# Optimization experiments

Measured on AMD Instinct MI355X. Metric: run time of the kernel, lower is better.

The kernel has to match this reference:

```python
import jax, jax.numpy as jnp
import numpy as np

IMG_W, IMG_H = 960.0, 512.0   # image_size (w, h)
HM_W, HM_H = 240, 128         # heatmap_size (w, h)


def _bilinear(fmap, gx, gy):
    # fmap: [C,H,W]; gx, gy: [N] normalized coords; bilinear, align_corners=False, zero padding
    C, H, W = fmap.shape
    ix = (gx + 1.0) * W * 0.5 - 0.5
    iy = (gy + 1.0) * H * 0.5 - 0.5
    x0f = jnp.floor(ix); y0f = jnp.floor(iy)
    wx1 = ix - x0f; wy1 = iy - y0f

    def tap(xf, yf, wgt):
        valid = (xf >= 0) & (xf <= W - 1) & (yf >= 0) & (yf <= H - 1)
        xc = jnp.clip(xf.astype(jnp.int32), 0, W - 1)
        yc = jnp.clip(yf.astype(jnp.int32), 0, H - 1)
        return fmap[:, yc, xc] * (wgt * valid.astype(fmap.dtype))

    return (tap(x0f, y0f, (1 - wx1) * (1 - wy1)) + tap(x0f + 1, y0f, wx1 * (1 - wy1))
            + tap(x0f, y0f + 1, (1 - wx1) * wy1) + tap(x0f + 1, y0f + 1, wx1 * wy1))


def _forward(feature_maps, grid_center, space_center, space_size, sub_space_size,
             cube, centers, trans, cam_R, cam_T, cam_f, cam_c):
    n_cam, B, C, H, W = feature_maps.shape
    vox = jnp.float32(cube)
    fine_n = (space_size / sub_space_size * (vox - 1.0)).astype(jnp.int32) + 1   # [3]
    fine_nf = fine_n.astype(jnp.float32)
    scale = (fine_nf - 1.0) / space_size
    bias = (-sub_space_size / 2.0 / space_size * (fine_nf - 1.0)
            - scale * (space_center - space_size / 2.0))
    centers_tl = jnp.round(grid_center[:, :3] * scale + bias).astype(jnp.int32)  # [B,3]
    offset = (centers_tl.astype(jnp.float32) / (fine_nf - 1.0) * space_size
              - space_size / 2.0 + sub_space_size / 2.0)                          # [B,3]
    mask_xy = jnp.maximum(((1.0 - grid_center[:, 5:7]) / 2.0 * (vox - 1.0)).astype(jnp.int32), 0)
    mask = jnp.concatenate([mask_xy, jnp.zeros((B, 1), jnp.int32)], axis=1)       # [B,3]
    start = jnp.maximum(centers_tl + mask, 0)
    end = jnp.minimum(centers_tl + cube - mask, fine_n)
    end = jnp.maximum(end, start + 1)

    # fixed-size sub-cube of fine-grid indices; out-of-window cells are masked to 0
    v = jnp.arange(cube)
    mesh = jnp.stack(jnp.meshgrid(v, v, v, indexing="ij"), axis=-1).reshape(-1, 3)  # [N,3]
    fidx = centers_tl[:, None, :] + mesh[None]                                       # [B,N,3]
    valid = jnp.all((fidx >= start[:, None, :]) & (fidx < end[:, None, :]), axis=-1)  # [B,N]
    valid = valid & (grid_center[:, 3:4] >= 0)
    world = (space_center - space_size / 2.0
             + fidx.astype(jnp.float32) / (fine_nf - 1.0) * space_size)              # [B,N,3]

    # pinhole world->pixel per (batch, camera)
    rel = world[:, None, :, :] - cam_T[:, :, None, :]                                # [B,K,N,3]
    Xc = jnp.einsum("bkij,bknj->bkni", cam_R, rel)
    xy = cam_f[:, :, None, :] * Xc[..., :2] / Xc[..., 2:3] + cam_c[:, :, None, :]    # [B,K,N,2]
    maxwh = jnp.max(centers * 2.0, axis=-1)[:, :, None, None]
    xy = jnp.clip(xy, -1.0, maxwh)
    xy = jnp.einsum("bkij,bknj->bkni", trans[..., :2], xy) + trans[:, :, None, :, 2]  # affine crop
    xy = xy * jnp.array([HM_W / IMG_W, HM_H / IMG_H], jnp.float32)
    g = jnp.clip(xy / jnp.array([HM_W - 1.0, HM_H - 1.0], jnp.float32) * 2.0 - 1.0, -1.1, 1.1)

    fm = jnp.transpose(feature_maps, (1, 0, 2, 3, 4))                                # [B,K,C,H,W]
    samp = jax.vmap(jax.vmap(_bilinear))(fm, g[..., 0], g[..., 1])                   # [B,K,C,N]
    samp = samp * valid[:, None, None, :].astype(samp.dtype)
    cubes = jnp.sum(samp, axis=1) / (n_cam + 1e-6)            # mean agg (bounding==1)
    cubes = jnp.clip(cubes, 0.0, 1.0).reshape(B, C, cube, cube, cube)
    return cubes, offset


def setup_inputs() -> dict:
    key = jax.random.key(0)
    ks = jax.random.split(key, 10)
    n_cam, B, C, H, W = 5, 4, 15, 128, 240
    feature_maps = jax.random.uniform(ks[0], (n_cam, B, C, H, W), jnp.float32)
    xy = jax.random.uniform(ks[1], (B, 2), minval=-3000.0, maxval=3000.0)
    z = jax.random.uniform(ks[2], (B, 1), minval=800.0, maxval=1200.0)
    flag = jnp.ones((B, 2), jnp.float32)  # cols 3 (validity >= 0) and 4
    m = jax.random.uniform(ks[3], (B, 2), minval=0.6, maxval=1.0)  # cols 5:7 mask fracs
    grid_center = jnp.concatenate([xy, z, flag, m], axis=1)        # [B,7]
    space_center = jnp.array([0.0, 0.0, 1000.0], jnp.float32)
    space_size = jnp.array([8000.0, 8000.0, 2000.0], jnp.float32)
    sub_space_size = jnp.array([2000.0, 2000.0, 2000.0], jnp.float32)
    centers = jnp.array([IMG_W / 2, IMG_H / 2], jnp.float32) + \
        jax.random.uniform(ks[4], (B, n_cam, 2), minval=-5.0, maxval=5.0)
    base = jnp.array([[1.0, 0.0, 0.0], [0.0, 1.0, 0.0]], jnp.float32)
    trans = base + 0.01 * jax.random.normal(ks[5], (B, n_cam, 2, 3), jnp.float32)
    cam_R = jnp.eye(3, dtype=jnp.float32) + 0.05 * jax.random.normal(ks[6], (B, n_cam, 3, 3), jnp.float32)
    t_xy = jax.random.uniform(ks[7], (B, n_cam, 2), minval=-500.0, maxval=500.0)
    cam_T = jnp.concatenate([t_xy, jnp.full((B, n_cam, 1), -6000.0, jnp.float32)], axis=-1)
    cam_f = jax.random.uniform(ks[8], (B, n_cam, 2), minval=500.0, maxval=700.0)
    cam_c = jnp.array([IMG_W / 2, IMG_H / 2], jnp.float32) + \
        jax.random.uniform(ks[9], (B, n_cam, 2), minval=-10.0, maxval=10.0)
    return {"feature_maps": feature_maps, "grid_center": grid_center,
            "space_center": space_center, "space_size": space_size,
            "sub_space_size": sub_space_size, "sub_cube_size": 64,
            "centers": centers, "trans": trans, "cam_R": cam_R,
            "cam_T": cam_T, "cam_f": cam_f, "cam_c": cam_c}


def reference(feature_maps, grid_center, space_center, space_size, sub_space_size,
              sub_cube_size, centers, trans, cam_R, cam_T, cam_f, cam_c):
    return _forward(feature_maps, grid_center, space_center, space_size, sub_space_size,
                    int(sub_cube_size), centers, trans, cam_R, cam_T, cam_f, cam_c)
```

## Files before the change

kernel.cpp:

```cpp
#include <hip/hip_runtime.h>
#include <hip/hip_fp16.h>

#define NCAM 5
#define NC 15
#define NCP 16
#define FH 128
#define FW 240
#define HW (FH*FW)
#define CUBE 64
#define NVOX (CUBE*CUBE*CUBE)
#define TTHREADS 256
#define MTHREADS 256
#define CSTR 24

__global__ __launch_bounds__(TTHREADS) void transpose_fm(
    const float* __restrict__ fm, __half* __restrict__ fmH,
    const float* __restrict__ gc, const float* __restrict__ space_c,
    const float* __restrict__ space_s, const float* __restrict__ sub_s,
    const float* __restrict__ centers, const float* __restrict__ trans,
    const float* __restrict__ cam_R, const float* __restrict__ cam_T,
    const float* __restrict__ cam_f, const float* __restrict__ cam_c,
    float* __restrict__ camS, int* __restrict__ bwin,
    float* __restrict__ out, int B)
{
    const int t = threadIdx.x;
    if (blockIdx.x == 0 && blockIdx.y == 0) {
        if (t < B) {
            const int b = t;
            #pragma unroll
            for (int d = 0; d < 3; ++d) {
                float ssz = space_s[d], sc = space_c[d], sub = sub_s[d];
                int   fn  = (int)(ssz / sub * (CUBE - 1.0f)) + 1;
                float fnf = (float)fn;
                float scale = (fnf - 1.0f) / ssz;
                float bias  = -sub / 2.0f / ssz * (fnf - 1.0f) - scale * (sc - ssz / 2.0f);
                int ctl = (int)rintf(gc[b*7 + d] * scale + bias);
                int mask = 0;
                if (d < 2) {
                    mask = (int)((1.0f - gc[b*7 + 5 + d]) / 2.0f * (CUBE - 1.0f));
                    if (mask < 0) mask = 0;
                }
                int st = max(ctl + mask, 0);
                int en = min(ctl + CUBE - mask, fn);
                en = max(en, st + 1);
                bwin[b*12 + d]     = ctl;
                bwin[b*12 + 3 + d] = st;
                bwin[b*12 + 6 + d] = en;
                out[(size_t)B * NC * NVOX + b*3 + d] =
                    (float)ctl / (fnf - 1.0f) * ssz - ssz / 2.0f + sub / 2.0f;
            }
            bwin[b*12 + 9] = (gc[b*7 + 3] >= 0.0f) ? 1 : 0;
        }
        if (t < B * NCAM) {
            const int bk = t;
            float sA[3], bA[3];
            #pragma unroll
            for (int d = 0; d < 3; ++d) {
                float ssz = space_s[d], sub = sub_s[d];
                int   fn  = (int)(ssz / sub * (CUBE - 1.0f)) + 1;
                sA[d] = ssz / ((float)fn - 1.0f);
                bA[d] = space_c[d] - ssz * 0.5f;
            }
            const float* R = cam_R + bk*9;
            const float* T = cam_T + bk*3;
            float* P = camS + (size_t)bk * CSTR;
            #pragma unroll
            for (int i = 0; i < 3; ++i) {
                #pragma unroll
                for (int d = 0; d < 3; ++d) P[i*3 + d] = R[i*3 + d] * sA[d];
                P[9 + i] = R[i*3+0]*(bA[0]-T[0]) + R[i*3+1]*(bA[1]-T[1]) + R[i*3+2]*(bA[2]-T[2]);
            }
            P[12] = cam_f[bk*2+0];  P[13] = cam_f[bk*2+1];
            P[14] = cam_c[bk*2+0];  P[15] = cam_c[bk*2+1];
            P[16] = fmaxf(centers[bk*2+0]*2.0f, centers[bk*2+1]*2.0f);
            const float* tr = trans + bk*6;
            const float KX = 60.0f/239.0f, KY = 32.0f/127.0f;
            P[17] = tr[0]*KX;  P[18] = tr[1]*KX;  P[19] = tr[2]*KX - 120.0f;
            P[20] = tr[3]*KY;  P[21] = tr[4]*KY;  P[22] = tr[5]*KY - 64.0f;
            P[23] = 0.0f;
        }
    }
    const int p  = blockIdx.x * TTHREADS + t;
    const int cb = blockIdx.y;
    const float* src = fm + (size_t)cb * NC * HW + p;
    __half v[NCP];
    #pragma unroll
    for (int c = 0; c < NC; ++c) v[c] = __float2half(src[(size_t)c * HW]);
    v[15] = __float2half(0.0f);
    uint4* dst = (uint4*)(fmH + ((size_t)cb * HW + p) * NCP);
    dst[0] = *(const uint4*)(v);
    dst[1] = *(const uint4*)(v + 8);
}

#define FMA_MIX2(lo, hi, wt, wrd)                                             \
    asm("v_fma_mix_f32 %0, %1, %2, %0 op_sel_hi:[0,1,0]"                      \
        : "+v"(lo) : "v"(wt), "v"(wrd));                                      \
    asm("v_fma_mix_f32 %0, %1, %2, %0 op_sel:[0,1,0] op_sel_hi:[0,1,0]"       \
        : "+v"(hi) : "v"(wt), "v"(wrd));

#define TAPFMA(wt, A, Bv)                                                     \
    FMA_MIX2(acc[0],  acc[1],  wt, A.x)                                       \
    FMA_MIX2(acc[2],  acc[3],  wt, A.y)                                       \
    FMA_MIX2(acc[4],  acc[5],  wt, A.z)                                       \
    FMA_MIX2(acc[6],  acc[7],  wt, A.w)                                       \
    FMA_MIX2(acc[8],  acc[9],  wt, Bv.x)                                      \
    FMA_MIX2(acc[10], acc[11], wt, Bv.y)                                      \
    FMA_MIX2(acc[12], acc[13], wt, Bv.z)                                      \
    asm("v_fma_mix_f32 %0, %1, %2, %0 op_sel_hi:[0,1,0]"                      \
        : "+v"(acc[14]) : "v"(wt), "v"(Bv.w));

__global__ __launch_bounds__(MTHREADS) void proj_main(
    const __half* __restrict__ fmH,
    const float* __restrict__ camS,
    const int* __restrict__ bwin,
    float* __restrict__ out, int B)
{
    const unsigned nwg = gridDim.x;
    const unsigned q = nwg >> 3, r = nwg & 7;
    const unsigned xcd = blockIdx.x & 7, idx = blockIdx.x >> 3;
    const unsigned wgid = (xcd < r ? xcd * (q + 1) : r * (q + 1) + (xcd - r) * q) + idx;

    const int b = wgid >> 10;
    const int n = (int)(wgid & 1023) * MTHREADS + threadIdx.x;
    const int vi = n >> 12, vj = (n >> 6) & 63, vk = n & 63;

    const int* W = bwin + b*12;
    const int fx = W[0] + vi, fy = W[1] + vj, fz = W[2] + vk;
    const bool valid = (fx >= W[3]) & (fx < W[6])
                     & (fy >= W[4]) & (fy < W[7])
                     & (fz >= W[5]) & (fz < W[8])
                     & (W[9] != 0);

    float acc[15];
    #pragma unroll
    for (int c = 0; c < 15; ++c) acc[c] = 0.0f;

    if (valid) {
        const float fxf = (float)fx, fyf = (float)fy, fzf = (float)fz;
        const float* cs = camS + (size_t)(b * NCAM) * CSTR;

        #pragma unroll
        for (int cam = 0; cam < NCAM; ++cam) {
            const float* P = cs + cam * CSTR;
            float X0 = fmaf(P[0], fxf, fmaf(P[1], fyf, fmaf(P[2], fzf, P[9])));
            float X1 = fmaf(P[3], fxf, fmaf(P[4], fyf, fmaf(P[5], fzf, P[10])));
            float X2 = fmaf(P[6], fxf, fmaf(P[7], fyf, fmaf(P[8], fzf, P[11])));
            float rz = __builtin_amdgcn_rcpf(X2);
            float px = fmaf(P[12]*X0, rz, P[14]);
            float py = fmaf(P[13]*X1, rz, P[15]);
            float mw = P[16];
            px = fminf(fmaxf(px, -1.0f), mw);
            py = fminf(fmaxf(py, -1.0f), mw);
            float ixf = fminf(fmaxf(fmaf(P[17], px, fmaf(P[18], py, P[19])), -132.0f), 132.0f) + 119.5f;
            float iyf = fminf(fmaxf(fmaf(P[20], px, fmaf(P[21], py, P[22])), -70.4f), 70.4f) + 63.5f;
            float x0f = floorf(ixf), y0f = floorf(iyf);
            float wx1 = ixf - x0f,  wy1 = iyf - y0f;
            float wx0 = 1.0f - wx1, wy0 = 1.0f - wy1;
            int x0 = (int)x0f, y0 = (int)y0f, x1 = x0 + 1, y1 = y0 + 1;
            bool vx0 = (unsigned)x0 <= (FW-1), vx1 = (unsigned)x1 <= (FW-1);
            bool vy0 = (unsigned)y0 <= (FH-1), vy1 = (unsigned)y1 <= (FH-1);
            float w0 = (vx0 && vy0) ? wx0*wy0 : 0.0f;
            float w1 = (vx1 && vy0) ? wx1*wy0 : 0.0f;
            float w2 = (vx0 && vy1) ? wx0*wy1 : 0.0f;
            float w3 = (vx1 && vy1) ? wx1*wy1 : 0.0f;
            int xc0 = min(max(x0,0),FW-1), xc1 = min(max(x1,0),FW-1);
            int yc0 = min(max(y0,0),FH-1), yc1 = min(max(y1,0),FH-1);

            const __half* bp = fmH + (size_t)(cam*B + b) * HW * NCP;
            const uint4* q0 = (const uint4*)(bp + (size_t)(yc0*FW + xc0) * NCP);
            const uint4* q1 = (const uint4*)(bp + (size_t)(yc0*FW + xc1) * NCP);
            const uint4* q2 = (const uint4*)(bp + (size_t)(yc1*FW + xc0) * NCP);
            const uint4* q3 = (const uint4*)(bp + (size_t)(yc1*FW + xc1) * NCP);
            uint4 a0 = q0[0], b0 = q0[1];
            uint4 a1 = q1[0], b1 = q1[1];
            uint4 a2 = q2[0], b2 = q2[1];
            uint4 a3 = q3[0], b3 = q3[1];

            TAPFMA(w0, a0, b0)
            TAPFMA(w1, a1, b1)
            TAPFMA(w2, a2, b2)
            TAPFMA(w3, a3, b3)
        }
    }

    const float RINV = 0.19999996000000800f;
    #pragma unroll
    for (int c = 0; c < NC; ++c) {
        float v = fminf(fmaxf(acc[c] * RINV, 0.0f), 1.0f);
        out[((size_t)(b*NC + c)) * NVOX + n] = v;
    }
}

__global__ __launch_bounds__(256) void proj_fallback(
    const float* __restrict__ fm, const float* __restrict__ gc,
    const float* __restrict__ space_center, const float* __restrict__ space_size,
    const float* __restrict__ sub_size, const float* __restrict__ centers,
    const float* __restrict__ trans, const float* __restrict__ cam_R,
    const float* __restrict__ cam_T, const float* __restrict__ cam_f,
    const float* __restrict__ cam_c, float* __restrict__ out, int B)
{
    const int b = blockIdx.x / (NVOX/256);
    const int n = (blockIdx.x % (NVOX/256)) * 256 + threadIdx.x;
    float ctlf[3], fnf[3], sc[3], ssz[3];
    int   ctl[3], st[3], en[3];
    #pragma unroll
    for (int d = 0; d < 3; ++d) {
        ssz[d] = space_size[d];
        sc[d]  = space_center[d];
        float sub = sub_size[d];
        int fn = (int)(ssz[d] / sub * (CUBE - 1.0f)) + 1;
        fnf[d] = (float)fn;
        float scale = (fnf[d] - 1.0f) / ssz[d];
        float bias  = -sub / 2.0f / ssz[d] * (fnf[d] - 1.0f)
                      - scale * (sc[d] - ssz[d] / 2.0f);
        int c_tl = (int)rintf(gc[b*7 + d] * scale + bias);
        ctl[d]  = c_tl;  ctlf[d] = (float)c_tl;
        int mask = 0;
        if (d < 2) {
            mask = (int)((1.0f - gc[b*7 + 5 + d]) / 2.0f * (CUBE - 1.0f));
            if (mask < 0) mask = 0;
        }
        st[d] = max(c_tl + mask, 0);
        int e = min(c_tl + CUBE - mask, fn);
        en[d] = max(e, st[d] + 1);
    }
    if (n < 3) {
        int d = n;
        out[(size_t)B * NC * NVOX + b*3 + d] =
            ctlf[d] / (fnf[d] - 1.0f) * ssz[d] - ssz[d] / 2.0f + sub_size[d] / 2.0f;
    }
    const int vi = n >> 12, vj = (n >> 6) & 63, vk = n & 63;
    const int fx = ctl[0] + vi, fy = ctl[1] + vj, fz = ctl[2] + vk;
    const bool valid = (fx >= st[0]) & (fx < en[0]) & (fy >= st[1]) & (fy < en[1])
                     & (fz >= st[2]) & (fz < en[2]) & (gc[b*7 + 3] >= 0.0f);
    float acc[NC];
    #pragma unroll
    for (int c = 0; c < NC; ++c) acc[c] = 0.0f;
    if (valid) {
        const float wxw = sc[0] - ssz[0]*0.5f + (float)fx / (fnf[0]-1.0f) * ssz[0];
        const float wyw = sc[1] - ssz[1]*0.5f + (float)fy / (fnf[1]-1.0f) * ssz[1];
        const float wzw = sc[2] - ssz[2]*0.5f + (float)fz / (fnf[2]-1.0f) * ssz[2];
        for (int cam = 0; cam < NCAM; ++cam) {
            const int bk = b*NCAM + cam;
            const float* R = cam_R + bk*9;
            const float* T = cam_T + bk*3;
            float r0 = wxw - T[0], r1 = wyw - T[1], r2 = wzw - T[2];
            float X0 = R[0]*r0 + R[1]*r1 + R[2]*r2;
            float X1 = R[3]*r0 + R[4]*r1 + R[5]*r2;
            float X2 = R[6]*r0 + R[7]*r1 + R[8]*r2;
            float px = cam_f[bk*2+0]*X0/X2 + cam_c[bk*2+0];
            float py = cam_f[bk*2+1]*X1/X2 + cam_c[bk*2+1];
            float maxwh = fmaxf(centers[bk*2+0]*2.0f, centers[bk*2+1]*2.0f);
            px = fminf(fmaxf(px, -1.0f), maxwh);
            py = fminf(fmaxf(py, -1.0f), maxwh);
            const float* tr = trans + bk*6;
            float tx = (tr[0]*px + tr[1]*py + tr[2]) * 0.25f;
            float ty = (tr[3]*px + tr[4]*py + tr[5]) * 0.25f;
            float gx = fminf(fmaxf(tx/239.0f*2.0f - 1.0f, -1.1f), 1.1f);
            float gy = fminf(fmaxf(ty/127.0f*2.0f - 1.0f, -1.1f), 1.1f);
            float ixf = (gx + 1.0f)*(FW*0.5f) - 0.5f;
            float iyf = (gy + 1.0f)*(FH*0.5f) - 0.5f;
            float x0f = floorf(ixf), y0f = floorf(iyf);
            float wx1 = ixf - x0f,  wy1 = iyf - y0f;
            float wx0 = 1.0f - wx1, wy0 = 1.0f - wy1;
            int x0 = (int)x0f, y0 = (int)y0f, x1 = x0 + 1, y1 = y0 + 1;
            bool vx0 = (x0 >= 0) & (x0 <= FW-1), vx1 = (x1 >= 0) & (x1 <= FW-1);
            bool vy0 = (y0 >= 0) & (y0 <= FH-1), vy1 = (y1 >= 0) & (y1 <= FH-1);
            float w00 = wx0*wy0*(float)(vx0 & vy0);
            float w10 = wx1*wy0*(float)(vx1 & vy0);
            float w01 = wx0*wy1*(float)(vx0 & vy1);
            float w11 = wx1*wy1*(float)(vx1 & vy1);
            int xc0 = min(max(x0,0),FW-1), xc1 = min(max(x1,0),FW-1);
            int yc0 = min(max(y0,0),FH-1), yc1 = min(max(y1,0),FH-1);
            int o00 = yc0*FW + xc0, o10 = yc0*FW + xc1;
            int o01 = yc1*FW + xc0, o11 = yc1*FW + xc1;
            const float* base = fm + ((size_t)(cam*B + b)) * NC * HW;
            #pragma unroll
            for (int c = 0; c < NC; ++c) {
                const float* p = base + c*HW;
                acc[c] += w00*p[o00] + w10*p[o10] + w01*p[o01] + w11*p[o11];
            }
        }
    }
    const float invd = (float)(5.0 + 1e-6);
    #pragma unroll
    for (int c = 0; c < NC; ++c) {
        float v = acc[c] / invd;
        v = fminf(fmaxf(v, 0.0f), 1.0f);
        out[((size_t)(b*NC + c)) * NVOX + n] = v;
    }
}

extern "C" void kernel_launch(void* const* d_in, const int* in_sizes, int n_in,
                              void* d_out, int out_size, void* d_ws, size_t ws_size,
                              hipStream_t stream) {
    const float* fm        = (const float*)d_in[0];
    const float* gc        = (const float*)d_in[1];
    const float* space_c   = (const float*)d_in[2];
    const float* space_s   = (const float*)d_in[3];
    const float* sub_s     = (const float*)d_in[4];
    const float* centers   = (const float*)d_in[6];
    const float* trans     = (const float*)d_in[7];
    const float* cam_R     = (const float*)d_in[8];
    const float* cam_T     = (const float*)d_in[9];
    const float* cam_f     = (const float*)d_in[10];
    const float* cam_c     = (const float*)d_in[11];
    float* out = (float*)d_out;
    const int B = in_sizes[1] / 7;

    const size_t FMHB   = (size_t)NCAM * B * HW * NCP * sizeof(__half);
    const size_t CAMOFF = (FMHB + 255) & ~(size_t)255;
    const size_t BWOFF  = (CAMOFF + (size_t)B * NCAM * CSTR * 4 + 255) & ~(size_t)255;
    const size_t NEED   = BWOFF + (size_t)B * 48;

    if (ws_size >= NEED) {
        __half* fmH  = (__half*)d_ws;
        float*  camS = (float*)((char*)d_ws + CAMOFF);
        int*    bwin = (int*)((char*)d_ws + BWOFF);
        dim3 tg(HW / TTHREADS, NCAM * B);
        hipLaunchKernelGGL(transpose_fm, tg, dim3(TTHREADS), 0, stream,
                           fm, fmH, gc, space_c, space_s, sub_s, centers, trans,
                           cam_R, cam_T, cam_f, cam_c, camS, bwin, out, B);
        dim3 grid(B * 1024), block(MTHREADS);
        hipLaunchKernelGGL(proj_main, grid, block, 0, stream,
                           fmH, camS, bwin, out, B);
    } else {
        dim3 grid(B * (NVOX/256)), block(256);
        hipLaunchKernelGGL(proj_fallback, grid, block, 0, stream,
                           fm, gc, space_c, space_s, sub_s,
                           centers, trans, cam_R, cam_T, cam_f, cam_c, out, B);
    }
}
```

Baseline: 40.07 us.

## Skip feature-map transpose outside each camera's projected sub-cube bounding box

```diff
diff --git a/kernel.cpp b/kernel.cpp
--- a/kernel.cpp
+++ b/kernel.cpp
@@ -24,9 +24,13 @@
     float* __restrict__ out, int B)
 {
     const int t = threadIdx.x;
+    const int cb = blockIdx.y;
+    const int cam = cb / B, b = cb - cam * B;
+    const int bk = b * NCAM + cam;
+
     if (blockIdx.x == 0 && blockIdx.y == 0) {
         if (t < B) {
-            const int b = t;
+            const int bb = t;
             #pragma unroll
             for (int d = 0; d < 3; ++d) {
                 float ssz = space_s[d], sc = space_c[d], sub = sub_s[d];
@@ -34,25 +38,25 @@
                 float fnf = (float)fn;
                 float scale = (fnf - 1.0f) / ssz;
                 float bias  = -sub / 2.0f / ssz * (fnf - 1.0f) - scale * (sc - ssz / 2.0f);
-                int ctl = (int)rintf(gc[b*7 + d] * scale + bias);
+                int ctl = (int)rintf(gc[bb*7 + d] * scale + bias);
                 int mask = 0;
                 if (d < 2) {
-                    mask = (int)((1.0f - gc[b*7 + 5 + d]) / 2.0f * (CUBE - 1.0f));
+                    mask = (int)((1.0f - gc[bb*7 + 5 + d]) / 2.0f * (CUBE - 1.0f));
                     if (mask < 0) mask = 0;
                 }
                 int st = max(ctl + mask, 0);
                 int en = min(ctl + CUBE - mask, fn);
                 en = max(en, st + 1);
-                bwin[b*12 + d]     = ctl;
-                bwin[b*12 + 3 + d] = st;
-                bwin[b*12 + 6 + d] = en;
-                out[(size_t)B * NC * NVOX + b*3 + d] =
+                bwin[bb*12 + d]     = ctl;
+                bwin[bb*12 + 3 + d] = st;
+                bwin[bb*12 + 6 + d] = en;
+                out[(size_t)B * NC * NVOX + bb*3 + d] =
                     (float)ctl / (fnf - 1.0f) * ssz - ssz / 2.0f + sub / 2.0f;
             }
-            bwin[b*12 + 9] = (gc[b*7 + 3] >= 0.0f) ? 1 : 0;
+            bwin[t*12 + 9] = (gc[t*7 + 3] >= 0.0f) ? 1 : 0;
         }
         if (t < B * NCAM) {
-            const int bk = t;
+            const int k = t;
             float sA[3], bA[3];
             #pragma unroll
             for (int d = 0; d < 3; ++d) {
@@ -61,27 +65,106 @@
                 sA[d] = ssz / ((float)fn - 1.0f);
                 bA[d] = space_c[d] - ssz * 0.5f;
             }
-            const float* R = cam_R + bk*9;
-            const float* T = cam_T + bk*3;
-            float* P = camS + (size_t)bk * CSTR;
+            const float* R = cam_R + k*9;
+            const float* T = cam_T + k*3;
+            float* P = camS + (size_t)k * CSTR;
             #pragma unroll
             for (int i = 0; i < 3; ++i) {
                 #pragma unroll
                 for (int d = 0; d < 3; ++d) P[i*3 + d] = R[i*3 + d] * sA[d];
                 P[9 + i] = R[i*3+0]*(bA[0]-T[0]) + R[i*3+1]*(bA[1]-T[1]) + R[i*3+2]*(bA[2]-T[2]);
             }
-            P[12] = cam_f[bk*2+0];  P[13] = cam_f[bk*2+1];
-            P[14] = cam_c[bk*2+0];  P[15] = cam_c[bk*2+1];
-            P[16] = fmaxf(centers[bk*2+0]*2.0f, centers[bk*2+1]*2.0f);
-            const float* tr = trans + bk*6;
+            P[12] = cam_f[k*2+0];  P[13] = cam_f[k*2+1];
+            P[14] = cam_c[k*2+0];  P[15] = cam_c[k*2+1];
+            P[16] = fmaxf(centers[k*2+0]*2.0f, centers[k*2+1]*2.0f);
+            const float* tr = trans + k*6;
             const float KX = 60.0f/239.0f, KY = 32.0f/127.0f;
             P[17] = tr[0]*KX;  P[18] = tr[1]*KX;  P[19] = tr[2]*KX - 120.0f;
             P[20] = tr[3]*KY;  P[21] = tr[4]*KY;  P[22] = tr[5]*KY - 64.0f;
             P[23] = 0.0f;
         }
     }
-    const int p  = blockIdx.x * TTHREADS + t;
-    const int cb = blockIdx.y;
+
+    float sA[3], bA[3];
+    #pragma unroll
+    for (int d = 0; d < 3; ++d) {
+        float ssz = space_s[d], sub = sub_s[d];
+        int fn = (int)(ssz / sub * (CUBE - 1.0f)) + 1;
+        sA[d] = ssz / ((float)fn - 1.0f);
+        bA[d] = space_c[d] - ssz * 0.5f;
+    }
+    const float* R = cam_R + bk*9;
+    const float* T = cam_T + bk*3;
+    float M[9], tv[3];
+    #pragma unroll
+    for (int i = 0; i < 3; ++i) {
+        #pragma unroll
+        for (int d = 0; d < 3; ++d) M[i*3+d] = R[i*3+d] * sA[d];
+        tv[i] = R[i*3+0]*(bA[0]-T[0]) + R[i*3+1]*(bA[1]-T[1]) + R[i*3+2]*(bA[2]-T[2]);
+    }
+    const float f0 = cam_f[bk*2+0], f1 = cam_f[bk*2+1];
+    const float c0 = cam_c[bk*2+0], c1 = cam_c[bk*2+1];
+    const float mw = fmaxf(centers[bk*2+0]*2.0f, centers[bk*2+1]*2.0f);
+    const float* tr = trans + bk*6;
+    const float KX = 60.0f/239.0f, KY = 32.0f/127.0f;
+    const float ax = tr[0]*KX, bx_ = tr[1]*KX, cxo = tr[2]*KX - 120.0f;
+    const float ay = tr[3]*KY, by_ = tr[4]*KY, cyo = tr[5]*KY - 64.0f;
+
+    float ctlf[3];
+    #pragma unroll
+    for (int d = 0; d < 3; ++d) {
+        float ssz = space_s[d], sc = space_c[d], sub = sub_s[d];
+        int fn = (int)(ssz / sub * (CUBE - 1.0f)) + 1;
+        float fnf = (float)fn;
+        float scale = (fnf - 1.0f) / ssz;
+        float bias = -sub/2.0f/ssz*(fnf-1.0f) - scale*(sc - ssz/2.0f);
+        ctlf[d] = rintf(gc[b*7+d]*scale + bias);
+    }
+
+    float pxmin = 1e30f, pxmax = -1e30f, pymin = 1e30f, pymax = -1e30f;
+    bool ok = true;
+    #pragma unroll
+    for (int ci = 0; ci < 8; ++ci) {
+        float vx = ctlf[0] + ((ci & 1) ? 63.0f : 0.0f);
+        float vy = ctlf[1] + ((ci & 2) ? 63.0f : 0.0f);
+        float vz = ctlf[2] + ((ci & 4) ? 63.0f : 0.0f);
+        float X0 = fmaf(M[0],vx, fmaf(M[1],vy, fmaf(M[2],vz, tv[0])));
+        float X1 = fmaf(M[3],vx, fmaf(M[4],vy, fmaf(M[5],vz, tv[1])));
+        float X2 = fmaf(M[6],vx, fmaf(M[7],vy, fmaf(M[8],vz, tv[2])));
+        ok = ok && (X2 > 1e-3f);
+        float rz = __builtin_amdgcn_rcpf(X2);
+        float px = fmaf(f0*X0, rz, c0);
+        float py = fmaf(f1*X1, rz, c1);
+        pxmin = fminf(pxmin, px); pxmax = fmaxf(pxmax, px);
+        pymin = fminf(pymin, py); pymax = fmaxf(pymax, py);
+    }
+    int bbx0, bbx1, bby0, bby1;
+    if (ok) {
+        float pxl = fminf(fmaxf(pxmin,-1.0f),mw), pxh = fminf(fmaxf(pxmax,-1.0f),mw);
+        float pyl = fminf(fmaxf(pymin,-1.0f),mw), pyh = fminf(fmaxf(pymax,-1.0f),mw);
+        float ixlo = (ax>0.f?ax*pxl:ax*pxh) + (bx_>0.f?bx_*pyl:bx_*pyh) + cxo;
+        float ixhi = (ax>0.f?ax*pxh:ax*pxl) + (bx_>0.f?bx_*pyh:bx_*pyl) + cxo;
+        ixlo = fminf(fmaxf(ixlo,-132.0f),132.0f) + 119.5f;
+        ixhi = fminf(fmaxf(ixhi,-132.0f),132.0f) + 119.5f;
+        float iylo = (ay>0.f?ay*pxl:ay*pxh) + (by_>0.f?by_*pyl:by_*pyh) + cyo;
+        float iyhi = (ay>0.f?ay*pxh:ay*pxl) + (by_>0.f?by_*pyh:by_*pyl) + cyo;
+        iylo = fminf(fmaxf(iylo,-70.4f),70.4f) + 63.5f;
+        iyhi = fminf(fmaxf(iyhi,-70.4f),70.4f) + 63.5f;
+        bbx0 = max((int)floorf(ixlo) - 1, 0);
+        bbx1 = min((int)floorf(ixhi) + 2, FW-1);
+        bby0 = max((int)floorf(iylo) - 1, 0);
+        bby1 = min((int)floorf(iyhi) + 2, FH-1);
+    } else {
+        bbx0 = 0; bbx1 = FW-1; bby0 = 0; bby1 = FH-1;
+    }
+
+    const int p0  = blockIdx.x * TTHREADS;
+    const int rlo = p0 / FW, rhi = (p0 + TTHREADS - 1) / FW;
+    if (rhi < bby0 || rlo > bby1) return;
+    const int p   = p0 + t;
+    const int pyy = p / FW, pxx = p - pyy * FW;
+    if (pyy < bby0 || pyy > bby1 || pxx < bbx0 || pxx > bbx1) return;
+
     const float* src = fm + (size_t)cb * NC * HW + p;
     __half v[NCP];
     #pragma unroll
```

Result: no change. 40.07 us (median of 2 runs) (+0.0%).
